# Optimization experiments

Hardware: AMD Instinct MI355X
Metric: run time of the kernel (lower is better)

Reference implementation:

```python
import jax, jax.numpy as jnp
import numpy as np
import math

B, N, D, H = 4, 2048, 1024, 16
DH = D // H  # dim per head
OUT = 1024

def setup_inputs() -> dict:
    key0 = jax.random.key(0)
    ks = jax.random.split(key0, 12)
    s = 1.0 / math.sqrt(D)
    return {
        "key": jax.random.normal(ks[0], (B, N, D), jnp.float32),
        "value": jax.random.normal(ks[1], (B, N, D), jnp.float32),
        "query": jax.random.normal(ks[2], (B, N, D), jnp.float32),
        "Wk": jax.random.normal(ks[3], (D, D), jnp.float32) * s,
        "bk": jax.random.normal(ks[4], (D,), jnp.float32) * 0.01,
        "Wv": jax.random.normal(ks[5], (D, D), jnp.float32) * s,
        "bv": jax.random.normal(ks[6], (D,), jnp.float32) * 0.01,
        "Wq": jax.random.normal(ks[7], (D, D), jnp.float32) * s,
        "bq": jax.random.normal(ks[8], (D,), jnp.float32) * 0.01,
        "Wo": jax.random.normal(ks[9], (D, OUT), jnp.float32) * s,
        "bo": jax.random.normal(ks[10], (OUT,), jnp.float32) * 0.01,
    }

def reference(key, value, query, Wk, bk, Wv, bv, Wq, bq, Wo, bo):
    scale = math.sqrt(DH)
    k = (key @ Wk + bk).reshape(B, N, H, DH).transpose(0, 2, 1, 3)    # [B,H,N,DH]
    v = (value @ Wv + bv).reshape(B, N, H, DH).transpose(0, 2, 1, 3)
    q = ((query @ Wq + bq) / scale).reshape(B, N, H, DH).transpose(0, 2, 1, 3)
    scores = jnp.einsum('bhqd,bhkd->bhqk', q, k).astype(jnp.float32)  # [B,H,N,N]
    attn = jax.nn.softmax(scores, axis=-1).astype(q.dtype)
    # dropout p=0.0 (eval / identity)
    ctx = jnp.einsum('bhqk,bhkd->bhqd', attn, v)                      # [B,H,N,DH]
    ctx = ctx.transpose(0, 2, 1, 3).reshape(B, N, D)
    out = ctx @ Wo + bo                                               # [B,N,OUT]
    return out
```

## Files before the change

kernel.cpp:

```cpp
#include <hip/hip_runtime.h>
#include <hip/hip_bf16.h>
#include <stdint.h>

#define BB 4
#define NN 2048
#define DD 1024
#define HH 16
#define DHH 64
#define MM (BB*NN)

typedef unsigned short u16;
typedef unsigned int u32;
typedef __bf16 bf16x8_t __attribute__((ext_vector_type(8)));
typedef float f32x4_t __attribute__((ext_vector_type(4)));
typedef float f32x16_t __attribute__((ext_vector_type(16)));

__device__ inline u16 f2b(float f) {
    __hip_bfloat16 h = __float2bfloat16(f);
    return *(u16*)&h;
}

__device__ inline u32 pack2(float lo, float hi) {
    __hip_bfloat162 h2 = __float22bfloat162_rn(make_float2(lo, hi));
    return *(u32*)&h2;
}

__device__ inline void gload16(const void* g, void* l) {
    __builtin_amdgcn_global_load_lds(
        (const __attribute__((address_space(1))) void*)g,
        (__attribute__((address_space(3))) void*)l, 16, 0, 0);
}

__global__ void cvt3_kernel(const float* __restrict__ in0, const float* __restrict__ in1,
                            const float* __restrict__ in2, u16* __restrict__ out0,
                            u16* __restrict__ out1, u16* __restrict__ out2) {
    const int z = blockIdx.y;
    const float* in = (z == 0) ? in0 : (z == 1) ? in1 : in2;
    u16* out = (z == 0) ? out0 : (z == 1) ? out1 : out2;
    int i = (blockIdx.x * 256 + threadIdx.x) * 4;
    float4 v = *(const float4*)(in + i);
    ushort4 o;
    o.x = f2b(v.x); o.y = f2b(v.y); o.z = f2b(v.z); o.w = f2b(v.w);
    *(ushort4*)(out + i) = o;
}

__global__ void wtrans_kernel(const float* __restrict__ W0, const float* __restrict__ W1,
                              const float* __restrict__ W2, const float* __restrict__ W3,
                              u16* __restrict__ out_base) {
    int z = blockIdx.z;
    const float* W = (z == 0) ? W0 : (z == 1) ? W1 : (z == 2) ? W2 : W3;
    u16* o = out_base + (size_t)z * DD * DD;
    __shared__ float tile[64][65];
    int t = threadIdx.x;
    int r0 = t >> 6;
    int c = t & 63;
    int kb = blockIdx.x, nb = blockIdx.y;
#pragma unroll
    for (int i = 0; i < 16; ++i) {
        int r = i * 4 + r0;
        tile[r][c] = W[(size_t)(kb * 64 + r) * DD + nb * 64 + c];
    }
    __syncthreads();
#pragma unroll
    for (int i = 0; i < 16; ++i) {
        int r = i * 4 + r0;
        o[(size_t)(nb * 64 + r) * DD + kb * 64 + c] = f2b(tile[c][r]);
    }
}

template<int OUT_F32, int BIAS_ROW>
__global__ __launch_bounds__(256, 2)
void gemm_bt(const u16* __restrict__ A, const u16* __restrict__ Bt,
             const float* __restrict__ bias, void* __restrict__ Cout, float scale,
             size_t a_z, size_t bt_z, size_t c_z, int ldc) {
    __shared__ u16 As[2][128 * 64];
    __shared__ u16 Bs[2][128 * 64];
    const int t = threadIdx.x;
    const int w = t >> 6, l = t & 63;
    const int wm = w >> 1, wn = w & 1;
    const int g = l >> 4, c = l & 15;
    const int bm = blockIdx.x, bn = blockIdx.y, z = blockIdx.z;
    A += (size_t)z * a_z;
    Bt += (size_t)z * bt_z;

    const f32x4_t vzero = {0.f, 0.f, 0.f, 0.f};
    f32x4_t acc[4][4];
#pragma unroll
    for (int m = 0; m < 4; ++m)
#pragma unroll
        for (int n = 0; n < 4; ++n) acc[m][n] = vzero;

    const int srow = l >> 3;
    const int scol = ((l & 7) ^ srow) << 3;
    const int sa = (l & 7) << 4;

    const u16* ap[4];
    const u16* bp[4];
#pragma unroll
    for (int i = 0; i < 4; ++i) {
        const int chunk = w * 4 + i, row = chunk * 8 + srow;
        ap[i] = A + (size_t)(bm * 128 + row) * DD + scol;
        bp[i] = Bt + (size_t)(bn * 128 + row) * DD + scol;
    }

#define GSTAGE(buf_)                                                         \
    do {                                                                     \
        _Pragma("unroll")                                                    \
        for (int i_ = 0; i_ < 4; ++i_) {                                     \
            gload16(ap[i_], &As[buf_][(w * 4 + i_) * 512]);                  \
            gload16(bp[i_], &Bs[buf_][(w * 4 + i_) * 512]);                  \
            ap[i_] += 64; bp[i_] += 64;                                      \
        }                                                                    \
    } while (0)

    GSTAGE(0);

#pragma unroll 1
    for (int ks = 0; ks < 16; ++ks) {
        const int cur = ks & 1;
        if (ks < 15) {
            GSTAGE(cur ^ 1);
            asm volatile("s_waitcnt vmcnt(8)" ::: "memory");
        } else {
            asm volatile("s_waitcnt vmcnt(0)" ::: "memory");
        }
        __builtin_amdgcn_s_barrier();
        asm volatile("" ::: "memory");

        bf16x8_t af[4][2], bfr[4][2];
#pragma unroll
        for (int m = 0; m < 4; ++m) {
            int rowa = wm * 64 + m * 16 + c;
#pragma unroll
            for (int kk = 0; kk < 2; ++kk)
                af[m][kk] = *(const bf16x8_t*)&As[cur][rowa * 64 + (((kk * 64 + g * 16) ^ sa) >> 1)];
        }
#pragma unroll
        for (int n = 0; n < 4; ++n) {
            int rowb = wn * 64 + n * 16 + c;
#pragma unroll
            for (int kk = 0; kk < 2; ++kk)
                bfr[n][kk] = *(const bf16x8_t*)&Bs[cur][rowb * 64 + (((kk * 64 + g * 16) ^ sa) >> 1)];
        }
        __builtin_amdgcn_s_setprio(1);
#pragma unroll
        for (int kk = 0; kk < 2; ++kk)
#pragma unroll
            for (int m = 0; m < 4; ++m)
#pragma unroll
                for (int n = 0; n < 4; ++n)
                    acc[m][n] = __builtin_amdgcn_mfma_f32_16x16x32_bf16(
                        af[m][kk], bfr[n][kk], acc[m][n], 0, 0, 0);
        __builtin_amdgcn_s_setprio(0);

        asm volatile("" ::: "memory");
        __builtin_amdgcn_s_barrier();
        asm volatile("" ::: "memory");
    }
#undef GSTAGE

    char* Cz = (char*)Cout + (size_t)z * c_z * (OUT_F32 ? 4 : 2);
#pragma unroll
    for (int n = 0; n < 4; ++n) {
        int col = bn * 128 + wn * 64 + n * 16 + c;
        float bcol = BIAS_ROW ? 0.f : bias[col];
#pragma unroll
        for (int m = 0; m < 4; ++m) {
            int row = bm * 128 + wm * 64 + m * 16 + g * 4;
            float4 brow;
            if (BIAS_ROW) brow = *(const float4*)&bias[row];
#pragma unroll
            for (int j = 0; j < 4; ++j) {
                float bv = BIAS_ROW ? ((const float*)&brow)[j] : bcol;
                float v = (acc[m][n][j] + bv) * scale;
                if (OUT_F32)
                    ((float*)Cz)[(size_t)(row + j) * ldc + col] = v;
                else
                    ((u16*)Cz)[(size_t)(row + j) * ldc + col] = f2b(v);
            }
        }
    }
}

__global__ __launch_bounds__(256, 2)
void attn32_kernel(const u16* __restrict__ qb, const u16* __restrict__ kb,
                   const u16* __restrict__ vt, u16* __restrict__ ctx) {
    __shared__ u16 Kt[4][64 * 64];
    __shared__ u16 Vs[4][64 * 64];
    const int t = threadIdx.x;
    const int w = t >> 6, l = t & 63;
    const int hl = l >> 5, l31 = l & 31, l7 = l & 7, l3 = l >> 3;

    const int f = blockIdx.y * 8 + blockIdx.x;
    const int wg = (f & 7) * 64 + (f >> 3);
    const int qt = wg & 7, bh = wg >> 3;
    const int b = bh >> 4, h = bh & 15;
    const int hoff = h * DHH;
    const size_t kv0 = (size_t)b * NN;
    const size_t vt0 = (size_t)bh * DHH;

    const size_t qrow_base = (size_t)(b * NN + qt * 256 + w * 64);
    bf16x8_t qf[2][4];
#pragma unroll
    for (int qm = 0; qm < 2; ++qm)
#pragma unroll
        for (int dks = 0; dks < 4; ++dks)
            qf[qm][dks] = *(const bf16x8_t*)&qb[(qrow_base + qm * 32 + l31) * DD +
                                                hoff + dks * 16 + hl * 8];

    f32x16_t z16;
#pragma unroll
    for (int r = 0; r < 16; ++r) z16[r] = 0.f;

    f32x16_t accO[2][2];
#pragma unroll
    for (int qm = 0; qm < 2; ++qm)
#pragma unroll
        for (int dt = 0; dt < 2; ++dt) accO[qm][dt] = z16;
    f32x16_t lacc16[2];
    lacc16[0] = z16; lacc16[1] = z16;

    const int scol2 = (l7 ^ l3) << 3;
    const u16* kp[2];
    const u16* vp[2];
#pragma unroll
    for (int i = 0; i < 2; ++i) {
        const int ch = w * 2 + i, r = ch * 8 + l3, rr = (r >> 2) & 3;
        const int pr = (rr == 1 || rr == 2) ? (r ^ 12) : r;
        kp[i] = kb + (kv0 + pr) * DD + hoff + scol2;
        vp[i] = vt + (vt0 + r) * NN + scol2;
    }

#define STAGE(S_)                                                            \
    do {                                                                     \
        _Pragma("unroll")                                                    \
        for (int i_ = 0; i_ < 2; ++i_) {                                     \
            gload16(kp[i_], &Kt[S_][(w * 2 + i_) * 512]);                    \
            gload16(vp[i_], &Vs[S_][(w * 2 + i_) * 512]);                    \
        }                                                                    \
        _Pragma("unroll")                                                    \
        for (int i_ = 0; i_ < 2; ++i_) { kp[i_] += 64 * DD; vp[i_] += 64; }  \
    } while (0)

    STAGE(0);
    STAGE(1);
    STAGE(2);

#pragma unroll 1
    for (int kt = 0; kt < NN / 64; ++kt) {
        const int cur = kt & 3;
        if (kt < NN / 64 - 3) {
            STAGE((kt + 3) & 3);
            asm volatile("s_waitcnt vmcnt(12)" ::: "memory");
        } else if (kt == NN / 64 - 3) {
            asm volatile("s_waitcnt vmcnt(8)" ::: "memory");
        } else if (kt == NN / 64 - 2) {
            asm volatile("s_waitcnt vmcnt(4)" ::: "memory");
        } else {
            asm volatile("s_waitcnt vmcnt(0)" ::: "memory");
        }
        __builtin_amdgcn_s_barrier();
        asm volatile("" ::: "memory");

        const char* Kc = (const char*)Kt[cur];
        const char* Vc = (const char*)Vs[cur];

        bf16x8_t kf[2][4];
#pragma unroll
        for (int kt32 = 0; kt32 < 2; ++kt32)
#pragma unroll
            for (int dks = 0; dks < 4; ++dks)
                kf[kt32][dks] = *(const bf16x8_t*)(Kc + (kt32 * 32 + l31) * 128 +
                                                   ((dks * 32 + hl * 16) ^ (l7 << 4)));

        f32x16_t accS[2][2];
        __builtin_amdgcn_s_setprio(1);
#pragma unroll
        for (int qm = 0; qm < 2; ++qm)
#pragma unroll
            for (int kt32 = 0; kt32 < 2; ++kt32) {
                accS[qm][kt32] = __builtin_amdgcn_mfma_f32_32x32x16_bf16(
                    kf[kt32][0], qf[qm][0], z16, 0, 0, 0);
#pragma unroll
                for (int dks = 1; dks < 4; ++dks)
                    accS[qm][kt32] = __builtin_amdgcn_mfma_f32_32x32x16_bf16(
                        kf[kt32][dks], qf[qm][dks], accS[qm][kt32], 0, 0, 0);
            }
        __builtin_amdgcn_s_setprio(0);

#pragma unroll
        for (int qm = 0; qm < 2; ++qm) {
#pragma unroll
            for (int kt32 = 0; kt32 < 2; ++kt32)
#pragma unroll
                for (int r = 0; r < 16; ++r)
                    accS[qm][kt32][r] = __builtin_amdgcn_exp2f(accS[qm][kt32][r]);
            lacc16[qm] += accS[qm][0] + accS[qm][1];
        }

        bf16x8_t vf[4][2];
#pragma unroll
        for (int pm = 0; pm < 4; ++pm)
#pragma unroll
            for (int dt = 0; dt < 2; ++dt)
                vf[pm][dt] = *(const bf16x8_t*)(Vc + (dt * 32 + l31) * 128 +
                                                ((pm * 32 + hl * 16) ^ (l7 << 4)));

        __builtin_amdgcn_s_setprio(1);
#pragma unroll
        for (int qm = 0; qm < 2; ++qm)
#pragma unroll
            for (int pm = 0; pm < 4; ++pm) {
                const int kt32 = pm >> 1, half = pm & 1;
                union { u32 u[4]; bf16x8_t v; } pu;
#pragma unroll
                for (int j2 = 0; j2 < 4; ++j2)
                    pu.u[j2] = pack2(accS[qm][kt32][half * 8 + 2 * j2],
                                     accS[qm][kt32][half * 8 + 2 * j2 + 1]);
#pragma unroll
                for (int dt = 0; dt < 2; ++dt)
                    accO[qm][dt] = __builtin_amdgcn_mfma_f32_32x32x16_bf16(
                        vf[pm][dt], pu.v, accO[qm][dt], 0, 0, 0);
            }
        __builtin_amdgcn_s_setprio(0);

        asm volatile("" ::: "memory");
        __builtin_amdgcn_s_barrier();
        asm volatile("" ::: "memory");
    }
#undef STAGE

#pragma unroll
    for (int qm = 0; qm < 2; ++qm) {
        float s8[8];
#pragma unroll
        for (int r = 0; r < 8; ++r) s8[r] = lacc16[qm][r] + lacc16[qm][r + 8];
#pragma unroll
        for (int sl = 4; sl >= 1; sl >>= 1)
#pragma unroll
            for (int r = 0; r < sl; ++r) s8[r] += s8[r + sl];
        float rsum = s8[0] + __shfl_xor(s8[0], 32);
        const float rl = 1.0f / rsum;
        const size_t qrow = qrow_base + qm * 32 + l31;
#pragma unroll
        for (int dt = 0; dt < 2; ++dt)
#pragma unroll
            for (int m = 0; m < 4; ++m) {
                ushort4 o;
                o.x = f2b(accO[qm][dt][4 * m + 0] * rl);
                o.y = f2b(accO[qm][dt][4 * m + 1] * rl);
                o.z = f2b(accO[qm][dt][4 * m + 2] * rl);
                o.w = f2b(accO[qm][dt][4 * m + 3] * rl);
                *(ushort4*)&ctx[qrow * DD + hoff + dt * 32 + m * 8 + hl * 4] = o;
            }
    }
}

extern "C" void kernel_launch(void* const* d_in, const int* in_sizes, int n_in,
                              void* d_out, int out_size, void* d_ws, size_t ws_size,
                              hipStream_t stream) {
    (void)in_sizes; (void)n_in; (void)out_size; (void)ws_size;
    const float* key   = (const float*)d_in[0];
    const float* value = (const float*)d_in[1];
    const float* query = (const float*)d_in[2];
    const float* Wk = (const float*)d_in[3];
    const float* bk = (const float*)d_in[4];
    const float* Wv = (const float*)d_in[5];
    const float* bv = (const float*)d_in[6];
    const float* Wq = (const float*)d_in[7];
    const float* bq = (const float*)d_in[8];
    const float* Wo = (const float*)d_in[9];
    const float* bo = (const float*)d_in[10];

    char* ws = (char*)d_ws;
    const size_t MB = 1024 * 1024;
    u16* vbf   = (u16*)(ws + 0 * MB);
    u16* kbf   = (u16*)(ws + 16 * MB);
    u16* qbf   = (u16*)(ws + 32 * MB);
    u16* VT    = (u16*)(ws + 48 * MB);
    u16* WtK   = (u16*)(ws + 64 * MB);
    u16* WtV   = (u16*)(ws + 66 * MB);
    u16* WtQ   = (u16*)(ws + 68 * MB);
    u16* WtO   = (u16*)(ws + 70 * MB);
    u16* kproj = vbf;
    u16* qproj = kbf;
    u16* ctx   = qbf;

    const int nelem = MM * DD;
    const int cvt_blocks = nelem / (256 * 4);

    wtrans_kernel<<<dim3(16, 16, 4), 256, 0, stream>>>(Wk, Wv, Wq, Wo, WtK);

    cvt3_kernel<<<dim3(cvt_blocks, 3), 256, 0, stream>>>(
        value, key, query, vbf, kbf, qbf);

    gemm_bt<0, 1><<<dim3(8, 16, 4), 256, 0, stream>>>(
        WtV, vbf, bv, VT, 1.0f, 0, (size_t)2048 * DD, (size_t)1024 * 2048, 2048);
    gemm_bt<0, 0><<<dim3(64, 8, 1), 256, 0, stream>>>(
        kbf, WtK, bk, kproj, 1.0f, 0, 0, 0, DD);
    gemm_bt<0, 0><<<dim3(64, 8, 1), 256, 0, stream>>>(
        qbf, WtQ, bq, qproj, 0.125f * 1.4426950408889634f, 0, 0, 0, DD);

    attn32_kernel<<<dim3(8, 64), 256, 0, stream>>>(qproj, kproj, VT, ctx);

    gemm_bt<1, 0><<<dim3(64, 8, 1), 256, 0, stream>>>(
        ctx, WtO, bo, d_out, 1.0f, 0, 0, 0, DD);
}
```

Baseline: 201.6 us.

## Fuse fp32-to-bf16 activation conversion into projection GEMM loads

Drops the standalone cvt3 kernel, which converted key, value and query to bf16 through a workspace round trip. The projection GEMMs now load fp32 activations straight into registers, pack them to bf16 and write them into swizzled LDS, software-pipelined two k-tiles ahead. The other operand still uses direct global-to-LDS loads. This saves a launch and roughly 100MB of traffic, at the cost of more registers, VALU packing work and fp32 reads from inside the GEMM (twice the bytes per tile on that side).

```diff
diff --git a/kernel.cpp b/kernel.cpp
--- a/kernel.cpp
+++ b/kernel.cpp
@@ -29,19 +29,6 @@
     __builtin_amdgcn_global_load_lds(
         (const __attribute__((address_space(1))) void*)g,
         (__attribute__((address_space(3))) void*)l, 16, 0, 0);
-}
-
-__global__ void cvt3_kernel(const float* __restrict__ in0, const float* __restrict__ in1,
-                            const float* __restrict__ in2, u16* __restrict__ out0,
-                            u16* __restrict__ out1, u16* __restrict__ out2) {
-    const int z = blockIdx.y;
-    const float* in = (z == 0) ? in0 : (z == 1) ? in1 : in2;
-    u16* out = (z == 0) ? out0 : (z == 1) ? out1 : out2;
-    int i = (blockIdx.x * 256 + threadIdx.x) * 4;
-    float4 v = *(const float4*)(in + i);
-    ushort4 o;
-    o.x = f2b(v.x); o.y = f2b(v.y); o.z = f2b(v.z); o.w = f2b(v.w);
-    *(ushort4*)(out + i) = o;
 }
 
 __global__ void wtrans_kernel(const float* __restrict__ W0, const float* __restrict__ W1,
@@ -68,9 +55,9 @@
     }
 }
 
-template<int OUT_F32, int BIAS_ROW>
+template<int OUT_F32, int BIAS_ROW, int F32SIDE>
 __global__ __launch_bounds__(256, 2)
-void gemm_bt(const u16* __restrict__ A, const u16* __restrict__ Bt,
+void gemm_bt(const void* __restrict__ Ap, const void* __restrict__ Btp,
              const float* __restrict__ bias, void* __restrict__ Cout, float scale,
              size_t a_z, size_t bt_z, size_t c_z, int ldc) {
     __shared__ u16 As[2][128 * 64];
@@ -80,8 +67,11 @@
     const int wm = w >> 1, wn = w & 1;
     const int g = l >> 4, c = l & 15;
     const int bm = blockIdx.x, bn = blockIdx.y, z = blockIdx.z;
-    A += (size_t)z * a_z;
-    Bt += (size_t)z * bt_z;
+
+    const u16* Ab = (const u16*)Ap + (size_t)z * (F32SIDE == 1 ? 0 : a_z);
+    const float* Af = (const float*)Ap + (size_t)z * (F32SIDE == 1 ? a_z : 0);
+    const u16* Bb = (const u16*)Btp + (size_t)z * (F32SIDE == 2 ? 0 : bt_z);
+    const float* Bf = (const float*)Btp + (size_t)z * (F32SIDE == 2 ? bt_z : 0);
 
     const f32x4_t vzero = {0.f, 0.f, 0.f, 0.f};
     f32x4_t acc[4][4];
@@ -99,30 +89,82 @@
 #pragma unroll
     for (int i = 0; i < 4; ++i) {
         const int chunk = w * 4 + i, row = chunk * 8 + srow;
-        ap[i] = A + (size_t)(bm * 128 + row) * DD + scol;
-        bp[i] = Bt + (size_t)(bn * 128 + row) * DD + scol;
-    }
-
-#define GSTAGE(buf_)                                                         \
+        if (F32SIDE != 1) ap[i] = Ab + (size_t)(bm * 128 + row) * DD + scol;
+        if (F32SIDE != 2) bp[i] = Bb + (size_t)(bn * 128 + row) * DD + scol;
+    }
+
+    const float* Fsrc = (F32SIDE == 1) ? Af : Bf;
+    const int fbase = (F32SIDE == 1) ? bm : bn;
+    float4 f0[4], f1[4];
+
+#define FLOAD(kt_)                                                           \
     do {                                                                     \
         _Pragma("unroll")                                                    \
         for (int i_ = 0; i_ < 4; ++i_) {                                     \
-            gload16(ap[i_], &As[buf_][(w * 4 + i_) * 512]);                  \
-            gload16(bp[i_], &Bs[buf_][(w * 4 + i_) * 512]);                  \
-            ap[i_] += 64; bp[i_] += 64;                                      \
+            const int tau_ = t + 256 * i_;                                   \
+            const int row_ = tau_ >> 3, cg_ = tau_ & 7;                      \
+            const float* gp_ = Fsrc + (size_t)(fbase * 128 + row_) * DD +    \
+                               (kt_)*64 + cg_ * 8;                           \
+            f0[i_] = *(const float4*)gp_;                                    \
+            f1[i_] = *(const float4*)(gp_ + 4);                              \
         }                                                                    \
     } while (0)
 
-    GSTAGE(0);
+#define FPACK(buf_)                                                          \
+    do {                                                                     \
+        u16* FS_ = (F32SIDE == 1) ? As[buf_] : Bs[buf_];                     \
+        _Pragma("unroll")                                                    \
+        for (int i_ = 0; i_ < 4; ++i_) {                                     \
+            const int tau_ = t + 256 * i_;                                   \
+            const int row_ = tau_ >> 3, cg_ = tau_ & 7;                      \
+            union { u32 u[4]; uint4 q; } pu_;                                \
+            pu_.u[0] = pack2(f0[i_].x, f0[i_].y);                            \
+            pu_.u[1] = pack2(f0[i_].z, f0[i_].w);                            \
+            pu_.u[2] = pack2(f1[i_].x, f1[i_].y);                            \
+            pu_.u[3] = pack2(f1[i_].z, f1[i_].w);                            \
+            *(uint4*)&FS_[row_ * 64 + ((cg_ ^ (row_ & 7)) << 3)] = pu_.q;    \
+        }                                                                    \
+    } while (0)
+
+#define STAGE_L(buf_)                                                        \
+    do {                                                                     \
+        _Pragma("unroll")                                                    \
+        for (int i_ = 0; i_ < 4; ++i_) {                                     \
+            if (F32SIDE != 1) {                                              \
+                gload16(ap[i_], &As[buf_][(w * 4 + i_) * 512]);              \
+                ap[i_] += 64;                                                \
+            }                                                                \
+            if (F32SIDE != 2) {                                              \
+                gload16(bp[i_], &Bs[buf_][(w * 4 + i_) * 512]);              \
+                bp[i_] += 64;                                                \
+            }                                                                \
+        }                                                                    \
+    } while (0)
+
+    if constexpr (F32SIDE != 0) {
+        FLOAD(0);
+        STAGE_L(0);
+        FPACK(0);
+        FLOAD(1);
+        asm volatile("s_waitcnt lgkmcnt(0)" ::: "memory");
+    } else {
+        STAGE_L(0);
+    }
 
 #pragma unroll 1
     for (int ks = 0; ks < 16; ++ks) {
         const int cur = ks & 1;
-        if (ks < 15) {
-            GSTAGE(cur ^ 1);
-            asm volatile("s_waitcnt vmcnt(8)" ::: "memory");
+        if (ks < 15) STAGE_L(cur ^ 1);
+        if constexpr (F32SIDE != 0) {
+            if (ks < 15)
+                asm volatile("s_waitcnt vmcnt(12) lgkmcnt(0)" ::: "memory");
+            else
+                asm volatile("s_waitcnt vmcnt(0) lgkmcnt(0)" ::: "memory");
         } else {
-            asm volatile("s_waitcnt vmcnt(0)" ::: "memory");
+            if (ks < 15)
+                asm volatile("s_waitcnt vmcnt(8)" ::: "memory");
+            else
+                asm volatile("s_waitcnt vmcnt(0)" ::: "memory");
         }
         __builtin_amdgcn_s_barrier();
         asm volatile("" ::: "memory");
@@ -156,8 +198,17 @@
         asm volatile("" ::: "memory");
         __builtin_amdgcn_s_barrier();
         asm volatile("" ::: "memory");
-    }
-#undef GSTAGE
+
+        if constexpr (F32SIDE != 0) {
+            if (ks < 15) {
+                FPACK(cur ^ 1);
+                if (ks < 14) FLOAD(ks + 2);
+            }
+        }
+    }
+#undef STAGE_L
+#undef FPACK
+#undef FLOAD
 
     char* Cz = (char*)Cout + (size_t)z * c_z * (OUT_F32 ? 4 : 2);
 #pragma unroll
@@ -374,35 +425,26 @@
 
     char* ws = (char*)d_ws;
     const size_t MB = 1024 * 1024;
-    u16* vbf   = (u16*)(ws + 0 * MB);
-    u16* kbf   = (u16*)(ws + 16 * MB);
-    u16* qbf   = (u16*)(ws + 32 * MB);
-    u16* VT    = (u16*)(ws + 48 * MB);
+    u16* kproj = (u16*)(ws + 0 * MB);
+    u16* qproj = (u16*)(ws + 16 * MB);
+    u16* VT    = (u16*)(ws + 32 * MB);
+    u16* ctx   = (u16*)(ws + 48 * MB);
     u16* WtK   = (u16*)(ws + 64 * MB);
     u16* WtV   = (u16*)(ws + 66 * MB);
     u16* WtQ   = (u16*)(ws + 68 * MB);
     u16* WtO   = (u16*)(ws + 70 * MB);
-    u16* kproj = vbf;
-    u16* qproj = kbf;
-    u16* ctx   = qbf;
-
-    const int nelem = MM * DD;
-    const int cvt_blocks = nelem / (256 * 4);
 
     wtrans_kernel<<<dim3(16, 16, 4), 256, 0, stream>>>(Wk, Wv, Wq, Wo, WtK);
 
-    cvt3_kernel<<<dim3(cvt_blocks, 3), 256, 0, stream>>>(
-        value, key, query, vbf, kbf, qbf);
-
-    gemm_bt<0, 1><<<dim3(8, 16, 4), 256, 0, stream>>>(
-        WtV, vbf, bv, VT, 1.0f, 0, (size_t)2048 * DD, (size_t)1024 * 2048, 2048);
-    gemm_bt<0, 0><<<dim3(64, 8, 1), 256, 0, stream>>>(
-        kbf, WtK, bk, kproj, 1.0f, 0, 0, 0, DD);
-    gemm_bt<0, 0><<<dim3(64, 8, 1), 256, 0, stream>>>(
-        qbf, WtQ, bq, qproj, 0.125f * 1.4426950408889634f, 0, 0, 0, DD);
+    gemm_bt<0, 1, 2><<<dim3(8, 16, 4), 256, 0, stream>>>(
+        WtV, value, bv, VT, 1.0f, 0, (size_t)2048 * DD, (size_t)1024 * 2048, 2048);
+    gemm_bt<0, 0, 1><<<dim3(64, 8, 1), 256, 0, stream>>>(
+        key, WtK, bk, kproj, 1.0f, 0, 0, 0, DD);
+    gemm_bt<0, 0, 1><<<dim3(64, 8, 1), 256, 0, stream>>>(
+        query, WtQ, bq, qproj, 0.125f * 1.4426950408889634f, 0, 0, 0, DD);
 
     attn32_kernel<<<dim3(8, 64), 256, 0, stream>>>(qproj, kproj, VT, ctx);
 
-    gemm_bt<1, 0><<<dim3(64, 8, 1), 256, 0, stream>>>(
+    gemm_bt<1, 0, 0><<<dim3(64, 8, 1), 256, 0, stream>>>(
         ctx, WtO, bo, d_out, 1.0f, 0, 0, 0, DD);
 }
```

After: 215.6 us. +7.0%, slower.
